# Optimization experiments

Measured on AMD Instinct MI355X. Metric: run time of the kernel, lower is better.

The kernel has to match this reference:

```python
import jax, jax.numpy as jnp
import numpy as np

T, H, I, E, K = 4096, 1024, 768, 8, 2

def setup_inputs() -> dict:
    key = jax.random.key(0)
    k1, k2, k3, k4 = jax.random.split(key, 4)
    s_h = 1.0 / np.sqrt(H)
    s_i = 1.0 / np.sqrt(I)
    return {
        "hidden_states": jax.random.normal(k1, (T, H), dtype=jnp.float32),
        "gate_w": jax.random.normal(k2, (E, H), dtype=jnp.float32) * s_h,   # router, fp32
        "w13": jax.random.normal(k3, (E, 2 * I, H), dtype=jnp.float32) * s_h,  # fused gate+up
        "w2": jax.random.normal(k4, (E, H, I), dtype=jnp.float32) * s_i,
        "num_global_tokens": T,
        "max_num_tokens_per_gpu": T,
    }

def reference(hidden_states, gate_w, w13, w2, num_global_tokens, max_num_tokens_per_gpu):
    x = hidden_states  # [T, H]
    orig_dtype = x.dtype
    # router runs in fp32 (router_dtype == 'float32')
    router_logits = jnp.einsum('th,eh->te', x.astype(jnp.float32), gate_w)
    router_logits = router_logits.astype(orig_dtype)
    # FusedMoE top-k: softmax in fp32 over all experts, then top-k; renormalize=False
    probs = jax.nn.softmax(router_logits.astype(jnp.float32), axis=-1)  # [T, E]
    topk_w, topk_ids = jax.lax.top_k(probs, K)  # [T, K]
    # dense combine weights [T, E] (scatter of top-k weights)
    combine = jnp.sum(jax.nn.one_hot(topk_ids, E, dtype=topk_w.dtype) * topk_w[..., None], axis=1)
    combine = combine.astype(orig_dtype)
    # dense per-expert SwiGLU MLP, masked-combined (grouped GEMM reference)
    h = jnp.einsum('th,ejh->tej', x, w13)  # [T, E, 2I]
    g, u = h[..., :I], h[..., I:]
    a = jax.nn.silu(g) * u                 # [T, E, I]
    o = jnp.einsum('tei,ehi->teh', a, w2)  # [T, E, H]
    out = jnp.einsum('teh,te->th', o, combine)  # routed_scaling_factor = 1.0
    return out.reshape(x.shape)
```

## Files before the change

kernel.cpp:

```cpp
#include <hip/hip_runtime.h>
#include <hip/hip_bf16.h>

#define TT 4096
#define HH 1024
#define II 768
#define EE 8
#define TWOI 1536

typedef __attribute__((ext_vector_type(8))) short bf16x8;
typedef __attribute__((ext_vector_type(4))) float f32x4;

__device__ unsigned short g_x_bf[TT * HH];
__device__ unsigned short g_w13_bf[EE * TWOI * HH];
__device__ unsigned short g_w2_bf[EE * HH * II];
__device__ unsigned short g_a[EE * TT * II];
__device__ float g_opart[2 * TT * HH];
__device__ int g_perm_tok[EE * TT];
__device__ float g_perm_w[EE * TT];
__device__ int g_perm_slot[EE * TT];
__device__ int g_cnt[EE];
__device__ int g_e1[TT];
__device__ int g_e2[TT];
__device__ float g_w1f[TT];
__device__ float g_w2f[TT];

__device__ __forceinline__ unsigned short f2bf(float f) {
  union { float f; unsigned u; } v; v.f = f;
  unsigned r = v.u + 0x7fff + ((v.u >> 16) & 1);
  return (unsigned short)(r >> 16);
}

__device__ __forceinline__ void gload16(const void* g, void* l) {
  __builtin_amdgcn_global_load_lds(
      (const __attribute__((address_space(1))) void*)g,
      (__attribute__((address_space(3))) void*)l, 16, 0, 0);
}

__device__ __forceinline__ void cvt_chunks(const float* __restrict__ in,
                                           unsigned short* __restrict__ dst,
                                           int nKB, int chunk) {
  const int lane = threadIdx.x & 63;
  const int r16 = lane & 15, c8 = lane >> 4;
  const int jbg = chunk / nKB, kb = chunk - jbg * nKB;
  const float* src = in + ((size_t)jbg * 16 + r16) * ((size_t)nKB * 32) + kb * 32 + c8 * 8;
  float4 v0 = *(const float4*)(src);
  float4 v1 = *(const float4*)(src + 4);
  ushort4 o0, o1;
  o0.x = f2bf(v0.x); o0.y = f2bf(v0.y); o0.z = f2bf(v0.z); o0.w = f2bf(v0.w);
  o1.x = f2bf(v1.x); o1.y = f2bf(v1.y); o1.z = f2bf(v1.z); o1.w = f2bf(v1.w);
  unsigned short* d = dst + (size_t)chunk * 512 + lane * 8;
  *(ushort4*)(d) = o0;
  *(ushort4*)(d + 4) = o1;
}

__global__ __launch_bounds__(256) void k_prep(const float* __restrict__ x,
                                              const float* __restrict__ gw) {
  const int b = blockIdx.x;
  const int wv = threadIdx.x >> 6;
  const int lane = threadIdx.x & 63;
  const int t = b * 4 + wv;

  const float* xr = x + (size_t)t * HH + lane * 16;
  float4 xv0 = *(const float4*)(xr + 0);
  float4 xv1 = *(const float4*)(xr + 4);
  float4 xv2 = *(const float4*)(xr + 8);
  float4 xv3 = *(const float4*)(xr + 12);

  unsigned short* xd = g_x_bf + (size_t)t * HH + lane * 16;
  ushort4 o0, o1, o2, o3;
  o0.x = f2bf(xv0.x); o0.y = f2bf(xv0.y); o0.z = f2bf(xv0.z); o0.w = f2bf(xv0.w);
  o1.x = f2bf(xv1.x); o1.y = f2bf(xv1.y); o1.z = f2bf(xv1.z); o1.w = f2bf(xv1.w);
  o2.x = f2bf(xv2.x); o2.y = f2bf(xv2.y); o2.z = f2bf(xv2.z); o2.w = f2bf(xv2.w);
  o3.x = f2bf(xv3.x); o3.y = f2bf(xv3.y); o3.z = f2bf(xv3.z); o3.w = f2bf(xv3.w);
  *(ushort4*)(xd + 0) = o0;
  *(ushort4*)(xd + 4) = o1;
  *(ushort4*)(xd + 8) = o2;
  *(ushort4*)(xd + 12) = o3;

  float lg[EE];
#pragma unroll
  for (int ei = 0; ei < EE; ++ei) {
    const float* gr = gw + ei * HH + lane * 16;
    float4 g0 = *(const float4*)(gr + 0);
    float4 g1 = *(const float4*)(gr + 4);
    float4 g2 = *(const float4*)(gr + 8);
    float4 g3 = *(const float4*)(gr + 12);
    float a = xv0.x * g0.x + xv0.y * g0.y + xv0.z * g0.z + xv0.w * g0.w
            + xv1.x * g1.x + xv1.y * g1.y + xv1.z * g1.z + xv1.w * g1.w
            + xv2.x * g2.x + xv2.y * g2.y + xv2.z * g2.z + xv2.w * g2.w
            + xv3.x * g3.x + xv3.y * g3.y + xv3.z * g3.z + xv3.w * g3.w;
#pragma unroll
    for (int s = 32; s > 0; s >>= 1) a += __shfl_xor(a, s);
    lg[ei] = a;
  }

  if (lane == 0) {
    float mx = lg[0];
#pragma unroll
    for (int ei = 1; ei < EE; ++ei) mx = fmaxf(mx, lg[ei]);
    float p[EE]; float s = 0.f;
#pragma unroll
    for (int ei = 0; ei < EE; ++ei) { p[ei] = expf(lg[ei] - mx); s += p[ei]; }
    float inv = 1.f / s;
    int e1 = 0; float b1 = lg[0];
#pragma unroll
    for (int ei = 1; ei < EE; ++ei) if (lg[ei] > b1) { b1 = lg[ei]; e1 = ei; }
    int e2 = -1; float b2 = -3.0e38f;
#pragma unroll
    for (int ei = 0; ei < EE; ++ei)
      if (ei != e1 && lg[ei] > b2) { b2 = lg[ei]; e2 = ei; }

    g_e1[t] = e1;
    g_e2[t] = e2;
    g_w1f[t] = p[e1] * inv;
    g_w2f[t] = p[e2] * inv;
  }
}

__global__ __launch_bounds__(256) void k_mid(const float* __restrict__ w13,
                                             const float* __restrict__ w2) {
  const int b = blockIdx.x;
  const int wv = threadIdx.x >> 6;
  if (b >= 8) {
    if (b < 6152) cvt_chunks(w13, g_w13_bf, 32, (b - 8) * 4 + wv);
    else          cvt_chunks(w2,  g_w2_bf,  24, (b - 6152) * 4 + wv);
    return;
  }
  const int e = b;
  const int tid = threadIdx.x;
  __shared__ int pre[256];

  const int t0 = tid * (TT / 256);
  int c = 0;
#pragma unroll
  for (int j = 0; j < TT / 256; ++j) {
    int t = t0 + j;
    if (g_e1[t] == e) ++c;
    if (g_e2[t] == e) ++c;
  }
  pre[tid] = c;
  __syncthreads();
  for (int off = 1; off < 256; off <<= 1) {
    int v = (tid >= off) ? pre[tid - off] : 0;
    __syncthreads();
    pre[tid] += v;
    __syncthreads();
  }
  int pos = pre[tid] - c;
#pragma unroll
  for (int j = 0; j < TT / 256; ++j) {
    int t = t0 + j;
    if (g_e1[t] == e) {
      g_perm_tok[e * TT + pos] = t;
      g_perm_w[e * TT + pos] = g_w1f[t];
      g_perm_slot[e * TT + pos] = 0;
      ++pos;
    }
    if (g_e2[t] == e) {
      g_perm_tok[e * TT + pos] = t;
      g_perm_w[e * TT + pos] = g_w2f[t];
      g_perm_slot[e * TT + pos] = 1;
      ++pos;
    }
  }
  if (tid == 255) g_cnt[e] = pre[255];
}

__global__ __launch_bounds__(512) void k_gemm1() {
  const int bid = blockIdx.x;
  const int e = bid & 7;
  const int k = bid >> 3;
  const int cb = k % 6;
  const int rowbase = (k / 6) * 128;
  const int cnt = g_cnt[e];
  if (rowbase >= cnt) return;
  const int tid = threadIdx.x;
  const int lane = tid & 63;
  const int wid = tid >> 6;
  const int wm = wid >> 1;
  const int wc = wid & 1;

  __shared__ uint4 sA[3][512];
  __shared__ uint4 sBg[3][512];
  __shared__ uint4 sBu[3][512];

  const int r16 = lane & 15;
  const int c8 = lane >> 4;
  const int arow = rowbase + wid * 16 + r16;
  const int tok = (arow < cnt) ? g_perm_tok[e * TT + arow] : 0;
  const unsigned short* aptr = g_x_bf + (size_t)tok * HH + c8 * 8;
  const unsigned short* bgp =
      g_w13_bf + ((size_t)(e * 96 + cb * 8 + wid) * 32) * 512 + lane * 8;
  const unsigned short* bup = bgp + (size_t)48 * 32 * 512;

  const int soff = __builtin_amdgcn_readfirstlane(wid * 1024);

#define STG1(buf, kk) do { \
    gload16(aptr + (kk) * 32, (char*)sA + (buf) * 8192 + soff); \
    gload16(bgp + (size_t)(kk) * 512, (char*)sBg + (buf) * 8192 + soff); \
    gload16(bup + (size_t)(kk) * 512, (char*)sBu + (buf) * 8192 + soff); \
  } while (0)

  f32x4 accg[2][4], accu[2][4];
#pragma unroll
  for (int m = 0; m < 2; ++m)
#pragma unroll
    for (int n = 0; n < 4; ++n) {
      accg[m][n] = (f32x4){0.f, 0.f, 0.f, 0.f};
      accu[m][n] = (f32x4){0.f, 0.f, 0.f, 0.f};
    }

  STG1(0, 0);
  STG1(1, 1);
  for (int ks = 0; ks < 32; ++ks) {
    const int cur = ks % 3;
    if (ks < 30) {
      const int stg = (ks + 2) % 3;
      STG1(stg, ks + 2);
      asm volatile("s_waitcnt vmcnt(6)" ::: "memory");
    } else if (ks == 30) {
      asm volatile("s_waitcnt vmcnt(3)" ::: "memory");
    } else {
      asm volatile("s_waitcnt vmcnt(0)" ::: "memory");
    }
    __builtin_amdgcn_s_barrier();
    __builtin_amdgcn_sched_barrier(0);
    bf16x8 af[2], bgf[4], buf_[4];
#pragma unroll
    for (int m = 0; m < 2; ++m)
      af[m] = *(const bf16x8*)((const char*)sA + cur * 8192 + (wm * 2 + m) * 1024 + lane * 16);
#pragma unroll
    for (int n = 0; n < 4; ++n) {
      int jb = wc * 4 + n;
      bgf[n] = *(const bf16x8*)((const char*)sBg + cur * 8192 + jb * 1024 + lane * 16);
      buf_[n] = *(const bf16x8*)((const char*)sBu + cur * 8192 + jb * 1024 + lane * 16);
    }
#pragma unroll
    for (int m = 0; m < 2; ++m)
#pragma unroll
      for (int n = 0; n < 4; ++n) {
        accg[m][n] = __builtin_amdgcn_mfma_f32_16x16x32_bf16(af[m], bgf[n], accg[m][n], 0, 0, 0);
        accu[m][n] = __builtin_amdgcn_mfma_f32_16x16x32_bf16(af[m], buf_[n], accu[m][n], 0, 0, 0);
      }
    __builtin_amdgcn_sched_barrier(0);
    __builtin_amdgcn_s_barrier();
  }
#undef STG1

  const int rhi = lane >> 4, clo = lane & 15;
  unsigned short* abase = g_a + ((size_t)(e * 256 + (rowbase >> 4)) * 24) * 512;
#pragma unroll
  for (int m = 0; m < 2; ++m) {
#pragma unroll
    for (int jj = 0; jj < 4; ++jj) {
      int rbl = wm * 2 + m;
      int rr = rhi * 4 + jj;
      int row = rowbase + rbl * 16 + rr;
      if (row < cnt) {
#pragma unroll
        for (int n = 0; n < 4; ++n) {
          int kb = cb * 4 + wc * 2 + (n >> 1);
          int sub = (2 * n + (clo >> 3)) & 3;
          float gv = accg[m][n][jj];
          float uv = accu[m][n][jj];
          float av = gv / (1.f + __expf(-gv)) * uv;
          abase[((size_t)rbl * 24 + kb) * 512 + sub * 128 + rr * 8 + (clo & 7)] = f2bf(av);
        }
      }
    }
  }
}

__global__ __launch_bounds__(512) void k_gemm2() {
  const int bid = blockIdx.x;
  const int e = bid & 7;
  const int k = bid >> 3;
  const int cb = k % 8;
  const int rowbase = (k / 8) * 128;
  const int cnt = g_cnt[e];
  if (rowbase >= cnt) return;
  const int tid = threadIdx.x;
  const int lane = tid & 63;
  const int wid = tid >> 6;
  const int wm = wid >> 1;
  const int wc = wid & 1;

  __shared__ uint4 sA[3][512];
  __shared__ uint4 sB[3][512];
  __shared__ int s_tok[128];
  __shared__ float s_w[128];
  __shared__ int s_slot[128];

  if (tid < 128) {
    int row = rowbase + tid;
    bool v = row < cnt;
    s_tok[tid] = v ? g_perm_tok[e * TT + row] : 0;
    s_w[tid] = v ? g_perm_w[e * TT + row] : 0.f;
    s_slot[tid] = v ? g_perm_slot[e * TT + row] : 0;
  }

  const unsigned short* aptr =
      g_a + ((size_t)(e * 256 + (rowbase >> 4) + wid) * 24) * 512 + lane * 8;
  const unsigned short* bp =
      g_w2_bf + ((size_t)(e * 64 + cb * 8 + wid) * 24) * 512 + lane * 8;

  const int soff = __builtin_amdgcn_readfirstlane(wid * 1024);

#define STG2(buf, kk) do { \
    gload16(aptr + (size_t)(kk) * 512, (char*)sA + (buf) * 8192 + soff); \
    gload16(bp + (size_t)(kk) * 512, (char*)sB + (buf) * 8192 + soff); \
  } while (0)

  f32x4 acc[2][4];
#pragma unroll
  for (int m = 0; m < 2; ++m)
#pragma unroll
    for (int n = 0; n < 4; ++n) acc[m][n] = (f32x4){0.f, 0.f, 0.f, 0.f};

  STG2(0, 0);
  STG2(1, 1);
  for (int ks = 0; ks < 24; ++ks) {
    const int cur = ks % 3;
    if (ks < 22) {
      const int stg = (ks + 2) % 3;
      STG2(stg, ks + 2);
      asm volatile("s_waitcnt vmcnt(4)" ::: "memory");
    } else if (ks == 22) {
      asm volatile("s_waitcnt vmcnt(2)" ::: "memory");
    } else {
      asm volatile("s_waitcnt vmcnt(0)" ::: "memory");
    }
    __builtin_amdgcn_s_barrier();
    __builtin_amdgcn_sched_barrier(0);
    bf16x8 af[2], bfr[4];
#pragma unroll
    for (int m = 0; m < 2; ++m)
      af[m] = *(const bf16x8*)((const char*)sA + cur * 8192 + (wm * 2 + m) * 1024 + lane * 16);
#pragma unroll
    for (int n = 0; n < 4; ++n)
      bfr[n] = *(const bf16x8*)((const char*)sB + cur * 8192 + (wc * 4 + n) * 1024 + lane * 16);
#pragma unroll
    for (int m = 0; m < 2; ++m)
#pragma unroll
      for (int n = 0; n < 4; ++n)
        acc[m][n] = __builtin_amdgcn_mfma_f32_16x16x32_bf16(af[m], bfr[n], acc[m][n], 0, 0, 0);
    __builtin_amdgcn_sched_barrier(0);
    __builtin_amdgcn_s_barrier();
  }
#undef STG2

  const int rhi = lane >> 4, clo = lane & 15;
#pragma unroll
  for (int m = 0; m < 2; ++m) {
#pragma unroll
    for (int jj = 0; jj < 4; ++jj) {
      int rloc = wm * 32 + m * 16 + rhi * 4 + jj;
      if (rowbase + rloc < cnt) {
        int tok = s_tok[rloc];
        float w = s_w[rloc];
        float* orow = g_opart + (size_t)s_slot[rloc] * TT * HH + (size_t)tok * HH;
#pragma unroll
        for (int n = 0; n < 4; ++n) {
          int h2 = cb * 128 + wc * 64 + n * 16 + clo;
          orow[h2] = w * acc[m][n][jj];
        }
      }
    }
  }
}

__global__ __launch_bounds__(256) void k_combine(float* __restrict__ out) {
  int idx = (blockIdx.x * 256 + threadIdx.x) * 4;
  float4 p0 = *(const float4*)(g_opart + idx);
  float4 p1 = *(const float4*)(g_opart + TT * HH + idx);
  float4 o;
  o.x = p0.x + p1.x; o.y = p0.y + p1.y; o.z = p0.z + p1.z; o.w = p0.w + p1.w;
  *(float4*)(out + idx) = o;
}

extern "C" void kernel_launch(void* const* d_in, const int* in_sizes, int n_in,
                              void* d_out, int out_size, void* d_ws, size_t ws_size,
                              hipStream_t stream) {
  (void)in_sizes; (void)n_in; (void)d_ws; (void)ws_size; (void)out_size;
  const float* x   = (const float*)d_in[0];
  const float* gw  = (const float*)d_in[1];
  const float* w13 = (const float*)d_in[2];
  const float* w2  = (const float*)d_in[3];
  float* out = (float*)d_out;

  k_prep<<<dim3(1024), dim3(256), 0, stream>>>(x, gw);
  k_mid<<<dim3(9224), dim3(256), 0, stream>>>(w13, w2);
  k_gemm1<<<dim3(480), dim3(512), 0, stream>>>();
  k_gemm2<<<dim3(640), dim3(512), 0, stream>>>();
  k_combine<<<dim3(TT * HH / 1024), dim3(256), 0, stream>>>(out);
}
```

Before: 114.5 us.

## Store MoE partial outputs in bf16 and move weight conversion into prep

Expert-output partials are now written as bf16 instead of fp32, which halves the write traffic in the second GEMM and the read traffic in the combine kernel. The combine kernel processes 8 elements per thread. Separately, the weight fp32-to-bf16 conversion blocks move from the compaction kernel into the prep kernel, so the routing compaction becomes a small 8-block launch. The cost is an extra bf16 rounding of the partial products before summation, which adds output error.

```diff
diff --git a/kernel.cpp b/kernel.cpp
--- a/kernel.cpp
+++ b/kernel.cpp
@@ -8,13 +8,14 @@
 #define TWOI 1536
 
 typedef __attribute__((ext_vector_type(8))) short bf16x8;
+typedef __attribute__((ext_vector_type(8))) unsigned short u16x8;
 typedef __attribute__((ext_vector_type(4))) float f32x4;
 
 __device__ unsigned short g_x_bf[TT * HH];
 __device__ unsigned short g_w13_bf[EE * TWOI * HH];
 __device__ unsigned short g_w2_bf[EE * HH * II];
 __device__ unsigned short g_a[EE * TT * II];
-__device__ float g_opart[2 * TT * HH];
+__device__ unsigned short g_opart[2 * TT * HH];
 __device__ int g_perm_tok[EE * TT];
 __device__ float g_perm_w[EE * TT];
 __device__ int g_perm_slot[EE * TT];
@@ -28,6 +29,10 @@
   union { float f; unsigned u; } v; v.f = f;
   unsigned r = v.u + 0x7fff + ((v.u >> 16) & 1);
   return (unsigned short)(r >> 16);
+}
+
+__device__ __forceinline__ float bf2f(unsigned short u) {
+  union { unsigned v; float f; } c; c.v = (unsigned)u << 16; return c.f;
 }
 
 __device__ __forceinline__ void gload16(const void* g, void* l) {
@@ -54,9 +59,16 @@
 }
 
 __global__ __launch_bounds__(256) void k_prep(const float* __restrict__ x,
-                                              const float* __restrict__ gw) {
+                                              const float* __restrict__ gw,
+                                              const float* __restrict__ w13,
+                                              const float* __restrict__ w2) {
   const int b = blockIdx.x;
   const int wv = threadIdx.x >> 6;
+  if (b >= 1024) {
+    if (b < 7168) cvt_chunks(w13, g_w13_bf, 32, (b - 1024) * 4 + wv);
+    else          cvt_chunks(w2,  g_w2_bf,  24, (b - 7168) * 4 + wv);
+    return;
+  }
   const int lane = threadIdx.x & 63;
   const int t = b * 4 + wv;
 
@@ -117,16 +129,8 @@
   }
 }
 
-__global__ __launch_bounds__(256) void k_mid(const float* __restrict__ w13,
-                                             const float* __restrict__ w2) {
-  const int b = blockIdx.x;
-  const int wv = threadIdx.x >> 6;
-  if (b >= 8) {
-    if (b < 6152) cvt_chunks(w13, g_w13_bf, 32, (b - 8) * 4 + wv);
-    else          cvt_chunks(w2,  g_w2_bf,  24, (b - 6152) * 4 + wv);
-    return;
-  }
-  const int e = b;
+__global__ __launch_bounds__(256) void k_compact() {
+  const int e = blockIdx.x;
   const int tid = threadIdx.x;
   __shared__ int pre[256];
 
@@ -358,11 +362,12 @@
       if (rowbase + rloc < cnt) {
         int tok = s_tok[rloc];
         float w = s_w[rloc];
-        float* orow = g_opart + (size_t)s_slot[rloc] * TT * HH + (size_t)tok * HH;
+        unsigned short* orow =
+            g_opart + (size_t)s_slot[rloc] * TT * HH + (size_t)tok * HH;
 #pragma unroll
         for (int n = 0; n < 4; ++n) {
           int h2 = cb * 128 + wc * 64 + n * 16 + clo;
-          orow[h2] = w * acc[m][n][jj];
+          orow[h2] = f2bf(w * acc[m][n][jj]);
         }
       }
     }
@@ -370,12 +375,20 @@
 }
 
 __global__ __launch_bounds__(256) void k_combine(float* __restrict__ out) {
-  int idx = (blockIdx.x * 256 + threadIdx.x) * 4;
-  float4 p0 = *(const float4*)(g_opart + idx);
-  float4 p1 = *(const float4*)(g_opart + TT * HH + idx);
-  float4 o;
-  o.x = p0.x + p1.x; o.y = p0.y + p1.y; o.z = p0.z + p1.z; o.w = p0.w + p1.w;
-  *(float4*)(out + idx) = o;
+  int idx = (blockIdx.x * 256 + threadIdx.x) * 8;
+  u16x8 p0 = *(const u16x8*)(g_opart + idx);
+  u16x8 p1 = *(const u16x8*)(g_opart + TT * HH + idx);
+  float4 o0, o1;
+  o0.x = bf2f(p0[0]) + bf2f(p1[0]);
+  o0.y = bf2f(p0[1]) + bf2f(p1[1]);
+  o0.z = bf2f(p0[2]) + bf2f(p1[2]);
+  o0.w = bf2f(p0[3]) + bf2f(p1[3]);
+  o1.x = bf2f(p0[4]) + bf2f(p1[4]);
+  o1.y = bf2f(p0[5]) + bf2f(p1[5]);
+  o1.z = bf2f(p0[6]) + bf2f(p1[6]);
+  o1.w = bf2f(p0[7]) + bf2f(p1[7]);
+  *(float4*)(out + idx) = o0;
+  *(float4*)(out + idx + 4) = o1;
 }
 
 extern "C" void kernel_launch(void* const* d_in, const int* in_sizes, int n_in,
@@ -388,9 +401,9 @@
   const float* w2  = (const float*)d_in[3];
   float* out = (float*)d_out;
 
-  k_prep<<<dim3(1024), dim3(256), 0, stream>>>(x, gw);
-  k_mid<<<dim3(9224), dim3(256), 0, stream>>>(w13, w2);
+  k_prep<<<dim3(10240), dim3(256), 0, stream>>>(x, gw, w13, w2);
+  k_compact<<<dim3(EE), dim3(256), 0, stream>>>();
   k_gemm1<<<dim3(480), dim3(512), 0, stream>>>();
   k_gemm2<<<dim3(640), dim3(512), 0, stream>>>();
-  k_combine<<<dim3(TT * HH / 1024), dim3(256), 0, stream>>>(out);
-}
+  k_combine<<<dim3(TT * HH / 2048), dim3(256), 0, stream>>>(out);
+}
```

Result: no change. 113.4 us (-1.0%).
